# Kernel tuning notes

Measured on AMD Instinct MI355X. Metric: run time of the kernel, lower is better.

## Reference

```python
import jax, jax.numpy as jnp
import numpy as np

NEG_INF = -9e15
ALPHA = 2.0  # LeakyReLU negative slope from init (alpha=2)


def setup_inputs() -> dict:
    key = jax.random.key(0)
    k1, k2, k3, k4 = jax.random.split(key, 4)
    B, N, Fin, Fout = 8, 2048, 256, 128
    x = jax.random.normal(k1, (B, N, Fin), dtype=jnp.float32)
    adj = jax.random.randint(k2, (B, N, N), 0, 2, dtype=jnp.int32)
    # xavier_uniform with gain=1.414
    def xavier(k, shape, gain=1.414):
        fan_in, fan_out = shape[0], shape[1]
        bound = gain * np.sqrt(6.0 / (fan_in + fan_out))
        return jax.random.uniform(k, shape, jnp.float32, -bound, bound)
    W = xavier(k3, (Fin, Fout))
    a = xavier(k4, (2 * Fout, 1))
    return {"x": x, "adj": adj, "W": W, "a": a}


def reference(x, adj, W, a):
    # Wh: [B, N, Fout]
    Wh = jnp.matmul(x, W)
    Fout = W.shape[1]
    a1 = a[:Fout, 0]   # [Fout]
    a2 = a[Fout:, 0]   # [Fout]
    f1 = jnp.einsum('bnf,f->bn', Wh, a1)  # [B, N]
    f2 = jnp.einsum('bnf,f->bn', Wh, a2)  # [B, N]
    e = f1[:, :, None] + f2[:, None, :]   # [B, N, N]
    e = jnp.where(e >= 0, e, ALPHA * e)   # leaky relu, slope 2
    e = jnp.where(adj > 0, e, NEG_INF)
    attention = jax.nn.softmax(e, axis=2)
    # dropout: eval mode (no-op)
    h_prime = jnp.matmul(attention, Wh)   # [B, N, Fout]
    # concat=True -> elu
    return jnp.where(h_prime > 0, h_prime, jnp.expm1(h_prime))
```

## Files before the change

### kernel.cpp

```cpp
#include <hip/hip_runtime.h>
#include <hip/hip_bf16.h>
#include <math.h>

constexpr int B_   = 8;
constexpr int N_   = 2048;
constexpr int FIN  = 256;
constexpr int FOUT = 128;

constexpr int CH  = 512;
constexpr int NCH = N_ / CH;
constexpr int PR  = CH + 8;
constexpr int XR  = FIN + 8;
constexpr int TR  = 40;

typedef __attribute__((ext_vector_type(8))) short bf16x8;
typedef __attribute__((ext_vector_type(4))) float f32x4;
typedef __attribute__((ext_vector_type(4))) int   i32x4;

static __device__ __forceinline__ unsigned short f2bf(float f) {
    __hip_bfloat16 h = __float2bfloat16(f);
    return *reinterpret_cast<unsigned short*>(&h);
}
static __device__ __forceinline__ i32x4 ntload4(const int* p) {
    return __builtin_nontemporal_load((const i32x4*)p);
}

__global__ __launch_bounds__(256) void k0_wt(const float* __restrict__ W,
                                             unsigned short* __restrict__ Wt) {
    const int n = blockIdx.x;
    const int k = threadIdx.x;
    Wt[n * FIN + k] = f2bf(W[k * FOUT + n]);
}

__global__ __launch_bounds__(256) void kp_mask(const int* __restrict__ adj,
                                               unsigned long long* __restrict__ maskW) {
    const int lane   = threadIdx.x & 63;
    const int wid    = (blockIdx.x * 256 + threadIdx.x) >> 6;
    const int nwaves = (2048 * 256) >> 6;
    const int ngrp   = (B_ * N_ * N_) / 256;

    for (int g = wid; g < ngrp; g += nwaves) {
        const int* base = adj + (size_t)g * 256 + 4 * lane;
        i32x4 v = ntload4(base);
        unsigned long long b0 = __ballot(v[0] > 0);
        unsigned long long b1 = __ballot(v[1] > 0);
        unsigned long long b2 = __ballot(v[2] > 0);
        unsigned long long b3 = __ballot(v[3] > 0);
        if (lane < 4) {
            unsigned long long w = (lane == 0) ? b0
                                 : (lane == 1) ? b1
                                 : (lane == 2) ? b2 : b3;
            maskW[(size_t)4 * g + lane] = w;
        }
    }
}

__global__ __launch_bounds__(256) void ka_wh(const float* __restrict__ x,
                                             const unsigned short* __restrict__ Wt,
                                             const float* __restrict__ a,
                                             unsigned short* __restrict__ WhT,
                                             float* __restrict__ f1,
                                             float* __restrict__ f2) {
    __shared__ unsigned short xs[32 * XR];
    __shared__ float as[2 * FOUT];
    __shared__ float fred[2][4][32];

    const int tid = threadIdx.x;
    const int j0  = blockIdx.x * 32;
    const int b   = j0 >> 11;
    const int jb  = j0 & (N_ - 1);

    if (tid < 2 * FOUT) as[tid] = a[tid];
    {
        const float4* xsrc = (const float4*)(x + (size_t)j0 * FIN);
#pragma unroll
        for (int t = 0; t < 8; ++t) {
            const int idx = tid + t * 256;
            float4 v = xsrc[idx];
            const int row = idx >> 6, c4 = idx & 63;
            ushort4 u;
            u.x = f2bf(v.x); u.y = f2bf(v.y); u.z = f2bf(v.z); u.w = f2bf(v.w);
            *(ushort4*)&xs[row * XR + c4 * 4] = u;
        }
    }
    __syncthreads();

    const int wave = tid >> 6, lane = tid & 63;
    const int quad = lane >> 4, l16 = lane & 15;

    f32x4 acc[2][2];
#pragma unroll
    for (int aa = 0; aa < 2; ++aa)
#pragma unroll
        for (int nn = 0; nn < 2; ++nn) acc[aa][nn] = {0.f, 0.f, 0.f, 0.f};

    const unsigned short* wtA0 = Wt + (size_t)(32 * wave + l16) * FIN;
    const unsigned short* wtA1 = wtA0 + 16 * FIN;
#pragma unroll
    for (int ks = 0; ks < FIN / 32; ++ks) {
        const int kof = ks * 32 + quad * 8;
        bf16x8 af0 = *(const bf16x8*)&wtA0[kof];
        bf16x8 af1 = *(const bf16x8*)&wtA1[kof];
        bf16x8 bf0 = *(const bf16x8*)&xs[l16 * XR + kof];
        bf16x8 bf1 = *(const bf16x8*)&xs[(16 + l16) * XR + kof];
        acc[0][0] = __builtin_amdgcn_mfma_f32_16x16x32_bf16(af0, bf0, acc[0][0], 0, 0, 0);
        acc[0][1] = __builtin_amdgcn_mfma_f32_16x16x32_bf16(af0, bf1, acc[0][1], 0, 0, 0);
        acc[1][0] = __builtin_amdgcn_mfma_f32_16x16x32_bf16(af1, bf0, acc[1][0], 0, 0, 0);
        acc[1][1] = __builtin_amdgcn_mfma_f32_16x16x32_bf16(af1, bf1, acc[1][1], 0, 0, 0);
    }
    __syncthreads();

    unsigned short* T = xs;
    float pf[2][2] = {{0.f, 0.f}, {0.f, 0.f}};
#pragma unroll
    for (int aa = 0; aa < 2; ++aa)
#pragma unroll
        for (int nn = 0; nn < 2; ++nn)
#pragma unroll
            for (int r = 0; r < 4; ++r) {
                const int d = 32 * wave + 16 * aa + 4 * quad + r;
                const float v = acc[aa][nn][r];
                T[d * TR + nn * 16 + l16] = f2bf(v);
                pf[0][nn] += v * as[d];
                pf[1][nn] += v * as[FOUT + d];
            }
#pragma unroll
    for (int ff = 0; ff < 2; ++ff)
#pragma unroll
        for (int nn = 0; nn < 2; ++nn) {
            float v = pf[ff][nn];
            v += __shfl_xor(v, 16);
            v += __shfl_xor(v, 32);
            pf[ff][nn] = v;
        }
    if (quad == 0) {
#pragma unroll
        for (int ff = 0; ff < 2; ++ff)
#pragma unroll
            for (int nn = 0; nn < 2; ++nn)
                fred[ff][wave][nn * 16 + l16] = pf[ff][nn];
    }
    __syncthreads();

    unsigned short* dstW = WhT + (size_t)b * FOUT * N_;
#pragma unroll
    for (int it = 0; it < 2; ++it) {
        const int idx = it * 256 + tid;
        const int d = idx >> 2, q = idx & 3;
        bf16x8 v = *(const bf16x8*)&T[d * TR + q * 8];
        *(bf16x8*)&dstW[(size_t)d * N_ + jb + q * 8] = v;
    }
    if (tid < 64) {
        const int ff = tid >> 5, j32 = tid & 31;
        const float s = fred[ff][0][j32] + fred[ff][1][j32] +
                        fred[ff][2][j32] + fred[ff][3][j32];
        (ff ? f2 : f1)[(size_t)b * N_ + jb + j32] = s;
    }
}

__global__ __launch_bounds__(512, 4) void kb_attn(const unsigned long long* __restrict__ maskW,
                                                  const unsigned short* __restrict__ WhT,
                                                  const float* __restrict__ f1,
                                                  const float* __restrict__ f2,
                                                  float* __restrict__ out) {
    __shared__ unsigned short p[2][16 * PR];
    __shared__ float rsum[16];

    const int tid  = threadIdx.x;
    const int b    = blockIdx.x & 7;
    const int i0   = (blockIdx.x >> 3) * 16;
    const int wave = tid >> 6, lane = tid & 63;
    const int quad = lane >> 4, l16 = lane & 15;

    const f32x4* f2b4 = (const f32x4*)(f2 + (size_t)b * N_);

    float f1r[2], s_run[2];
#pragma unroll
    for (int rr = 0; rr < 2; ++rr) {
        f1r[rr]   = f1[(size_t)b * N_ + i0 + wave * 2 + rr];
        s_run[rr] = 0.f;
    }

    f32x4 acc = {0.f, 0.f, 0.f, 0.f};
    const unsigned short* wBr =
        WhT + (size_t)b * FOUT * N_ + (size_t)(wave * 16 + l16) * N_;

    auto PROCESS = [&](int c) {
        unsigned short* pb = &p[c & 1][0];
        const f32x4 fva = f2b4[c * (CH / 4) + lane];
        const f32x4 fvb = f2b4[c * (CH / 4) + 64 + lane];
#pragma unroll
        for (int rr = 0; rr < 2; ++rr) {
            const int ti = wave * 2 + rr;
            const float f1i = f1r[rr];
            const size_t gbase =
                (((size_t)b * N_ + (size_t)(i0 + ti)) * N_ + (size_t)c * CH) >> 8;
            const unsigned long long* mw = maskW + 4 * gbase;
            const unsigned long long m00 = mw[0], m01 = mw[1];
            const unsigned long long m02 = mw[2], m03 = mw[3];
            const unsigned long long m10 = mw[4], m11 = mw[5];
            const unsigned long long m12 = mw[6], m13 = mw[7];

            float e[8];
            e[0] = f1i + fva[0]; e[1] = f1i + fva[1];
            e[2] = f1i + fva[2]; e[3] = f1i + fva[3];
            e[4] = f1i + fvb[0]; e[5] = f1i + fvb[1];
            e[6] = f1i + fvb[2]; e[7] = f1i + fvb[3];
#pragma unroll
            for (int q = 0; q < 8; ++q) e[q] = (e[q] >= 0.f) ? e[q] : 2.f * e[q];

            float pv[8];
            pv[0] = ((m00 >> lane) & 1ull) ? __expf(e[0]) : 0.f;
            pv[1] = ((m01 >> lane) & 1ull) ? __expf(e[1]) : 0.f;
            pv[2] = ((m02 >> lane) & 1ull) ? __expf(e[2]) : 0.f;
            pv[3] = ((m03 >> lane) & 1ull) ? __expf(e[3]) : 0.f;
            pv[4] = ((m10 >> lane) & 1ull) ? __expf(e[4]) : 0.f;
            pv[5] = ((m11 >> lane) & 1ull) ? __expf(e[5]) : 0.f;
            pv[6] = ((m12 >> lane) & 1ull) ? __expf(e[6]) : 0.f;
            pv[7] = ((m13 >> lane) & 1ull) ? __expf(e[7]) : 0.f;

            s_run[rr] += ((pv[0] + pv[1]) + (pv[2] + pv[3])) +
                         ((pv[4] + pv[5]) + (pv[6] + pv[7]));

            ushort4 u0, u1;
            u0.x = f2bf(pv[0]); u0.y = f2bf(pv[1]);
            u0.z = f2bf(pv[2]); u0.w = f2bf(pv[3]);
            u1.x = f2bf(pv[4]); u1.y = f2bf(pv[5]);
            u1.z = f2bf(pv[6]); u1.w = f2bf(pv[7]);
            *(ushort4*)&pb[ti * PR + 4 * lane]       = u0;
            *(ushort4*)&pb[ti * PR + 256 + 4 * lane] = u1;
        }
    };

    PROCESS(0);
    __syncthreads();

    for (int c = 0; c < NCH; ++c) {
        if (c + 1 < NCH) {
            PROCESS(c + 1);
        } else {
#pragma unroll
            for (int rr = 0; rr < 2; ++rr) {
                float s = s_run[rr];
#pragma unroll
                for (int o = 32; o; o >>= 1) s += __shfl_xor(s, o);
                if (lane == 0) rsum[wave * 2 + rr] = s;
            }
        }

        const unsigned short* wBc = wBr + (size_t)c * CH;
        const unsigned short* pA = &p[c & 1][l16 * PR];
#pragma unroll
        for (int ks = 0; ks < CH / 32; ++ks) {
            bf16x8 bfr = *(const bf16x8*)&wBc[ks * 32 + quad * 8];
            bf16x8 afr = *(const bf16x8*)&pA[ks * 32 + quad * 8];
            acc = __builtin_amdgcn_mfma_f32_16x16x32_bf16(afr, bfr, acc,
                                                          0, 0, 0);
        }
        __syncthreads();
    }

#pragma unroll
    for (int r = 0; r < 4; ++r) {
        const int m = quad * 4 + r;
        const float inv = 1.f / rsum[m];
        float v = acc[r] * inv;
        v = (v > 0.f) ? v : expm1f(v);
        out[((size_t)b * N_ + i0 + m) * FOUT + wave * 16 + l16] = v;
    }
}

extern "C" void kernel_launch(void* const* d_in, const int* in_sizes, int n_in,
                              void* d_out, int out_size, void* d_ws, size_t ws_size,
                              hipStream_t stream) {
    const float* x   = (const float*)d_in[0];
    const int*   adj = (const int*)d_in[1];
    const float* W   = (const float*)d_in[2];
    const float* a   = (const float*)d_in[3];
    float* out = (float*)d_out;

    unsigned short* WhT = (unsigned short*)d_ws;
    unsigned short* Wt  = WhT + (size_t)B_ * FOUT * N_;
    float* f1 = (float*)(Wt + (size_t)FOUT * FIN);
    float* f2 = f1 + (size_t)B_ * N_;
    unsigned long long* maskW = (unsigned long long*)(f2 + (size_t)B_ * N_);

    hipLaunchKernelGGL(k0_wt, dim3(FOUT), dim3(FIN), 0, stream, W, Wt);
    hipLaunchKernelGGL(kp_mask, dim3(2048), dim3(256), 0, stream, adj, maskW);
    hipLaunchKernelGGL(ka_wh, dim3(B_ * N_ / 32), dim3(256), 0, stream,
                       x, Wt, a, WhT, f1, f2);
    hipLaunchKernelGGL(kb_attn, dim3(B_ * N_ / 16), dim3(512), 0, stream,
                       maskW, WhT, f1, f2, out);
}
```

Measured before the change: 277.3 us.

## Fuse weight transpose into mask packing and store Wh in MFMA fragment order

Merges the W transpose kernel into the adjacency bitmask packing kernel, removing one launch. The mask packer now has each wave handle 16 fixed groups and issues four nontemporal loads per batch, replacing the grid-stride loop, to increase memory-level parallelism. Wh is written in a fragment-ordered layout so that each lane's B-operand load in the attention kernel reads contiguous 16-byte chunks, where the old layout used rows strided by N. The attention-stage gather becomes coalesced, at the cost of more complex, scattered stores in the Wh kernel.

```diff
diff --git a/kernel.cpp b/kernel.cpp
--- a/kernel.cpp
+++ b/kernel.cpp
@@ -25,32 +25,36 @@
     return __builtin_nontemporal_load((const i32x4*)p);
 }
 
-__global__ __launch_bounds__(256) void k0_wt(const float* __restrict__ W,
-                                             unsigned short* __restrict__ Wt) {
-    const int n = blockIdx.x;
-    const int k = threadIdx.x;
-    Wt[n * FIN + k] = f2bf(W[k * FOUT + n]);
-}
-
-__global__ __launch_bounds__(256) void kp_mask(const int* __restrict__ adj,
+__global__ __launch_bounds__(256) void k0_pack(const float* __restrict__ W,
+                                               unsigned short* __restrict__ Wt,
+                                               const int* __restrict__ adj,
                                                unsigned long long* __restrict__ maskW) {
-    const int lane   = threadIdx.x & 63;
-    const int wid    = (blockIdx.x * 256 + threadIdx.x) >> 6;
-    const int nwaves = (2048 * 256) >> 6;
-    const int ngrp   = (B_ * N_ * N_) / 256;
-
-    for (int g = wid; g < ngrp; g += nwaves) {
-        const int* base = adj + (size_t)g * 256 + 4 * lane;
-        i32x4 v = ntload4(base);
-        unsigned long long b0 = __ballot(v[0] > 0);
-        unsigned long long b1 = __ballot(v[1] > 0);
-        unsigned long long b2 = __ballot(v[2] > 0);
-        unsigned long long b3 = __ballot(v[3] > 0);
-        if (lane < 4) {
-            unsigned long long w = (lane == 0) ? b0
-                                 : (lane == 1) ? b1
-                                 : (lane == 2) ? b2 : b3;
-            maskW[(size_t)4 * g + lane] = w;
+    const int tid  = threadIdx.x;
+    const int lane = tid & 63, wv = tid >> 6;
+
+    if (blockIdx.x < FOUT) {
+        Wt[blockIdx.x * FIN + tid] = f2bf(W[tid * FOUT + blockIdx.x]);
+    }
+
+    const int gbase = blockIdx.x * 64 + wv * 16;
+    for (int t0 = 0; t0 < 16; t0 += 4) {
+        i32x4 vv[4];
+#pragma unroll
+        for (int u = 0; u < 4; ++u)
+            vv[u] = ntload4(adj + (size_t)(gbase + t0 + u) * 256 + 4 * lane);
+#pragma unroll
+        for (int u = 0; u < 4; ++u) {
+            const int g = gbase + t0 + u;
+            unsigned long long b0 = __ballot(vv[u][0] > 0);
+            unsigned long long b1 = __ballot(vv[u][1] > 0);
+            unsigned long long b2 = __ballot(vv[u][2] > 0);
+            unsigned long long b3 = __ballot(vv[u][3] > 0);
+            if (lane < 4) {
+                unsigned long long w = (lane == 0) ? b0
+                                     : (lane == 1) ? b1
+                                     : (lane == 2) ? b2 : b3;
+                maskW[(size_t)4 * g + lane] = w;
+            }
         }
     }
 }
@@ -58,7 +62,7 @@
 __global__ __launch_bounds__(256) void ka_wh(const float* __restrict__ x,
                                              const unsigned short* __restrict__ Wt,
                                              const float* __restrict__ a,
-                                             unsigned short* __restrict__ WhT,
+                                             unsigned short* __restrict__ Whf,
                                              float* __restrict__ f1,
                                              float* __restrict__ f2) {
     __shared__ unsigned short xs[32 * XR];
@@ -142,13 +146,14 @@
     }
     __syncthreads();
 
-    unsigned short* dstW = WhT + (size_t)b * FOUT * N_;
+    unsigned short* dstW = Whf + (size_t)(b * 8) * 256 * 128;
+    const int jb8 = jb >> 3;
 #pragma unroll
     for (int it = 0; it < 2; ++it) {
-        const int idx = it * 256 + tid;
-        const int d = idx >> 2, q = idx & 3;
-        bf16x8 v = *(const bf16x8*)&T[d * TR + q * 8];
-        *(bf16x8*)&dstW[(size_t)d * N_ + jb + q * 8] = v;
+        const int i   = it * 256 + tid;
+        const int n16 = i & 15, q = (i >> 4) & 3, nt = i >> 6;
+        bf16x8 v = *(const bf16x8*)&T[(nt * 16 + n16) * TR + q * 8];
+        *(bf16x8*)&dstW[((size_t)nt * 256 + jb8 + q) * 128 + n16 * 8] = v;
     }
     if (tid < 64) {
         const int ff = tid >> 5, j32 = tid & 31;
@@ -159,7 +164,7 @@
 }
 
 __global__ __launch_bounds__(512, 4) void kb_attn(const unsigned long long* __restrict__ maskW,
-                                                  const unsigned short* __restrict__ WhT,
+                                                  const unsigned short* __restrict__ Whf,
                                                   const float* __restrict__ f1,
                                                   const float* __restrict__ f2,
                                                   float* __restrict__ out) {
@@ -182,8 +187,8 @@
     }
 
     f32x4 acc = {0.f, 0.f, 0.f, 0.f};
-    const unsigned short* wBr =
-        WhT + (size_t)b * FOUT * N_ + (size_t)(wave * 16 + l16) * N_;
+    const unsigned short* wAll =
+        Whf + ((size_t)(b * 8 + wave) * 256) * 128 + quad * 128 + l16 * 8;
 
     auto PROCESS = [&](int c) {
         unsigned short* pb = &p[c & 1][0];
@@ -248,11 +253,11 @@
             }
         }
 
-        const unsigned short* wBc = wBr + (size_t)c * CH;
+        const unsigned short* wBc = wAll + (size_t)c * (64 * 128);
         const unsigned short* pA = &p[c & 1][l16 * PR];
 #pragma unroll
         for (int ks = 0; ks < CH / 32; ++ks) {
-            bf16x8 bfr = *(const bf16x8*)&wBc[ks * 32 + quad * 8];
+            bf16x8 bfr = *(const bf16x8*)&wBc[ks * 512];
             bf16x8 afr = *(const bf16x8*)&pA[ks * 32 + quad * 8];
             acc = __builtin_amdgcn_mfma_f32_16x16x32_bf16(afr, bfr, acc,
                                                           0, 0, 0);
@@ -279,16 +284,16 @@
     const float* a   = (const float*)d_in[3];
     float* out = (float*)d_out;
 
-    unsigned short* WhT = (unsigned short*)d_ws;
-    unsigned short* Wt  = WhT + (size_t)B_ * FOUT * N_;
+    unsigned short* Whf = (unsigned short*)d_ws;
+    unsigned short* Wt  = Whf + (size_t)B_ * FOUT * N_;
     float* f1 = (float*)(Wt + (size_t)FOUT * FIN);
     float* f2 = f1 + (size_t)B_ * N_;
     unsigned long long* maskW = (unsigned long long*)(f2 + (size_t)B_ * N_);
 
-    hipLaunchKernelGGL(k0_wt, dim3(FOUT), dim3(FIN), 0, stream, W, Wt);
-    hipLaunchKernelGGL(kp_mask, dim3(2048), dim3(256), 0, stream, adj, maskW);
+    hipLaunchKernelGGL(k0_pack, dim3(2048), dim3(256), 0, stream,
+                       W, Wt, adj, maskW);
     hipLaunchKernelGGL(ka_wh, dim3(B_ * N_ / 32), dim3(256), 0, stream,
-                       x, Wt, a, WhT, f1, f2);
+                       x, Wt, a, Whf, f1, f2);
     hipLaunchKernelGGL(kb_attn, dim3(B_ * N_ / 16), dim3(512), 0, stream,
-                       maskW, WhT, f1, f2, out);
-}
+                       maskW, Whf, f1, f2, out);
+}
```

Measured after the change: 236.2 us. 1.17x faster.
